# Optimization experiments

Hardware: AMD Instinct MI355X
Metric: run time of the kernel (lower is better)

Reference implementation:

```python
import jax, jax.numpy as jnp
import numpy as np

R = 16
ALPHA = 32
SCALING = ALPHA / R
SLOTS = 32
IN_F = 4096
OUT_F = 4096
B, T = 8, 1024


def setup_inputs() -> dict:
    key = jax.random.key(0)
    k1, k2, k3, k4, k5, k6 = jax.random.split(key, 6)
    x = jax.random.normal(k1, (B, T, IN_F), dtype=jnp.float32)
    adapter_mapping = jax.random.randint(k2, (B,), 0, SLOTS, dtype=jnp.int32)
    W = jax.random.normal(k3, (OUT_F, IN_F), dtype=jnp.float32) * 0.02
    b = jax.random.normal(k4, (OUT_F,), dtype=jnp.float32) * 0.02
    lora_As = jax.random.normal(k5, (SLOTS, IN_F, R), dtype=jnp.float32) * 0.02
    lora_Bs = jax.random.normal(k6, (SLOTS, R, OUT_F), dtype=jnp.float32) * 0.02
    return {"x": x, "adapter_mapping": adapter_mapping, "W": W, "b": b,
            "lora_As": lora_As, "lora_Bs": lora_Bs}


def reference(x, adapter_mapping, W, b, lora_As, lora_Bs):
    # base linear: y = x @ W.T + b
    base_out = jnp.einsum('bti,oi->bto', x, W) + b
    # per-example adapter gather (index_select along slot dim)
    A = lora_As[adapter_mapping]          # [B, in, r]
    Bm = lora_Bs[adapter_mapping]         # [B, r, out]
    lora_h = jnp.einsum('bti,bir->btr', x, A)
    lora_out = jnp.einsum('btr,bro->bto', lora_h, Bm)
    return base_out + lora_out * SCALING
```

## Files before the change

### kernel.cpp

```cpp
#include <hip/hip_runtime.h>
#include <hip/hip_bf16.h>


typedef __bf16 bf16_t;
typedef __bf16 bf16x8 __attribute__((ext_vector_type(8)));
typedef __bf16 bf16x4 __attribute__((ext_vector_type(4)));
typedef float f32x4 __attribute__((ext_vector_type(4)));

#define M_DIM 8192
#define K_DIM 4096
#define N_DIM 4096
#define SCALE_F 2.0f

#define LORA_BLOCKS 256
#define CVT_BLOCKS 2048
#define PREP_BLOCKS (LORA_BLOCKS + CVT_BLOCKS)

__device__ __forceinline__ void gload_lds16(const void* g, void* l) {
    __builtin_amdgcn_global_load_lds(
        (const __attribute__((address_space(1))) void*)g,
        (__attribute__((address_space(3))) void*)l, 16, 0, 0);
}

__global__ __launch_bounds__(256) void prep_kernel(
    const float* __restrict__ X,
    const float* __restrict__ lora_As,
    const int* __restrict__ mapping,
    float* __restrict__ h_ws,
    bf16_t* __restrict__ Xb,
    const float* __restrict__ W,
    bf16_t* __restrict__ Wb)
{
    __shared__ bf16_t Xt[32 * 16 * 8];
    __shared__ bf16_t At[16 * 136];
    __shared__ float hred[4 * 2 * 16 * 16];

    const int tid = threadIdx.x;
    const int bid = blockIdx.x;

    if (bid >= LORA_BLOCKS) {
        if (Wb) {
            const int n4 = N_DIM * K_DIM / 4;
            int i = (bid - LORA_BLOCKS) * 256 + tid;
            const int stride = CVT_BLOCKS * 256;
            for (; i < n4; i += stride) {
                f32x4 v = ((const f32x4*)W)[i];
                bf16x4 o = {(bf16_t)v[0], (bf16_t)v[1], (bf16_t)v[2], (bf16_t)v[3]};
                ((bf16x4*)Wb)[i] = o;
            }
        }
        return;
    }

    const int wave = tid >> 6;
    const int lane = tid & 63;
    const int bm0  = bid * 32;
    const int slot = mapping[bm0 >> 10];
    const float* __restrict__ A = lora_As + (size_t)slot * (K_DIM * 16);

    const int srow = tid >> 3;
    const int sc2  = tid & 7;
    const int r16  = lane & 15;
    const int kq   = lane >> 4;
    const int kk   = tid >> 1;
    const int half = tid & 1;

    f32x4 acc[2];
    acc[0] = (f32x4){0.f, 0.f, 0.f, 0.f};
    acc[1] = (f32x4){0.f, 0.f, 0.f, 0.f};

    const float* xrow = X + (size_t)(bm0 + srow) * K_DIM + sc2 * 16;

    f32x4 xv0 = *(const f32x4*)(xrow);
    f32x4 xv1 = *(const f32x4*)(xrow + 4);
    f32x4 xv2 = *(const f32x4*)(xrow + 8);
    f32x4 xv3 = *(const f32x4*)(xrow + 12);
    f32x4 av0 = *(const f32x4*)(A + (size_t)kk * 16 + half * 8);
    f32x4 av1 = *(const f32x4*)(A + (size_t)kk * 16 + half * 8 + 4);

    for (int k0 = 0; k0 < K_DIM; k0 += 128) {
        bf16x8 c0 = {(bf16_t)xv0[0], (bf16_t)xv0[1], (bf16_t)xv0[2], (bf16_t)xv0[3],
                     (bf16_t)xv1[0], (bf16_t)xv1[1], (bf16_t)xv1[2], (bf16_t)xv1[3]};
        bf16x8 c1 = {(bf16_t)xv2[0], (bf16_t)xv2[1], (bf16_t)xv2[2], (bf16_t)xv2[3],
                     (bf16_t)xv3[0], (bf16_t)xv3[1], (bf16_t)xv3[2], (bf16_t)xv3[3]};
        if (Xb) {
            bf16x8* xbp = (bf16x8*)(Xb + (size_t)(bm0 + srow) * K_DIM + k0 + sc2 * 16);
            xbp[0] = c0;
            xbp[1] = c1;
        }
        const int k8a = sc2 * 2, k8b = sc2 * 2 + 1;
        *(bf16x8*)(Xt + (srow * 16 + (k8a ^ (srow & 15))) * 8) = c0;
        *(bf16x8*)(Xt + (srow * 16 + (k8b ^ (srow & 15))) * 8) = c1;

#pragma unroll
        for (int rr = 0; rr < 4; ++rr) {
            At[(half * 8 + rr) * 136 + kk]     = (bf16_t)av0[rr];
            At[(half * 8 + 4 + rr) * 136 + kk] = (bf16_t)av1[rr];
        }
        __syncthreads();

        if (k0 + 128 < K_DIM) {
            const float* xp = xrow + k0 + 128;
            xv0 = *(const f32x4*)(xp);
            xv1 = *(const f32x4*)(xp + 4);
            xv2 = *(const f32x4*)(xp + 8);
            xv3 = *(const f32x4*)(xp + 12);
            const float* ap = A + (size_t)(k0 + 128 + kk) * 16 + half * 8;
            av0 = *(const f32x4*)ap;
            av1 = *(const f32x4*)(ap + 4);
        }

#pragma unroll
        for (int i = 0; i < 2; ++i) {
            const int row_l = i * 16 + r16;
            const int c = wave * 4 + kq;
            bf16x8 af  = *(const bf16x8*)(Xt + (row_l * 16 + (c ^ (row_l & 15))) * 8);
            bf16x8 bfr = *(const bf16x8*)(At + r16 * 136 + wave * 32 + kq * 8);
            acc[i] = __builtin_amdgcn_mfma_f32_16x16x32_bf16(af, bfr, acc[i], 0, 0, 0);
        }
        __syncthreads();
    }

#pragma unroll
    for (int i = 0; i < 2; ++i)
#pragma unroll
        for (int e = 0; e < 4; ++e)
            hred[wave * 512 + i * 256 + (kq * 4 + e) * 16 + r16] = acc[i][e];
    __syncthreads();
#pragma unroll
    for (int q = 0; q < 2; ++q) {
        const int entry = tid * 2 + q;
        const int row_l = entry >> 4, col = entry & 15;
        const int i = row_l >> 4, rr = row_l & 15;
        const int off = i * 256 + rr * 16 + col;
        float s = hred[off] + hred[512 + off] + hred[1024 + off] + hred[1536 + off];
        h_ws[(size_t)(bm0 + row_l) * 16 + col] = s * SCALE_F;
    }
}

__device__ __forceinline__ void epilogue(
    f32x4 (&acc)[4][4], const float* __restrict__ bias,
    const float* __restrict__ lora_Bs, const int* __restrict__ mapping,
    const float* __restrict__ h_ws, float* __restrict__ out,
    int bm0, int bn0, int wm0, int wn0, int r16, int kq)
{
    const int slot = mapping[bm0 >> 10];
    const bool hasK = (kq < 2);
    const int kq2 = hasK ? kq : 0;

    bf16x8 hfrag[4], bmf[4];
#pragma unroll
    for (int i = 0; i < 4; ++i) {
        const float* hp = h_ws + (size_t)(bm0 + wm0 + i * 16 + r16) * 16 + kq2 * 8;
        f32x4 h0 = *(const f32x4*)hp;
        f32x4 h1 = *(const f32x4*)(hp + 4);
#pragma unroll
        for (int jj = 0; jj < 4; ++jj) {
            hfrag[i][jj]     = hasK ? (bf16_t)h0[jj] : (bf16_t)0.f;
            hfrag[i][jj + 4] = hasK ? (bf16_t)h1[jj] : (bf16_t)0.f;
        }
    }
#pragma unroll
    for (int j = 0; j < 4; ++j) {
        const int o = bn0 + wn0 + j * 16 + r16;
#pragma unroll
        for (int jj = 0; jj < 8; ++jj) {
            const int r = kq2 * 8 + jj;
            const float v = lora_Bs[((size_t)slot * 16 + r) * N_DIM + o];
            bmf[j][jj] = hasK ? (bf16_t)v : (bf16_t)0.f;
        }
    }
#pragma unroll
    for (int i = 0; i < 4; ++i)
#pragma unroll
        for (int j = 0; j < 4; ++j)
            acc[i][j] = __builtin_amdgcn_mfma_f32_16x16x32_bf16(hfrag[i], bmf[j], acc[i][j], 0, 0, 0);

#pragma unroll
    for (int j = 0; j < 4; ++j) {
        const int o = bn0 + wn0 + j * 16 + r16;
        const float bv = bias[o];
#pragma unroll
        for (int i = 0; i < 4; ++i) {
#pragma unroll
            for (int e = 0; e < 4; ++e) {
                const int m = bm0 + wm0 + i * 16 + kq * 4 + e;
                out[(size_t)m * N_DIM + o] = acc[i][j][e] + bv;
            }
        }
    }
}

__global__ __launch_bounds__(256) void gemm_lora_direct(
    const bf16_t* __restrict__ Xb, const bf16_t* __restrict__ Wb,
    const float* __restrict__ bias, const float* __restrict__ lora_Bs,
    const int* __restrict__ mapping, const float* __restrict__ h_ws,
    float* __restrict__ out)
{
    __shared__ bf16_t As[128 * 64];
    __shared__ bf16_t Bs[128 * 64];

    const int tid  = threadIdx.x;
    const int wave = tid >> 6;
    const int lane = tid & 63;
    const int bid  = blockIdx.x;
    const int n_t  = (bid & 7) + ((bid >> 9) << 3);
    const int m_t  = (bid >> 3) & 63;
    const int bm0 = m_t * 128;
    const int bn0 = n_t * 128;
    const int wm0 = (wave >> 1) * 64;
    const int wn0 = (wave & 1) * 64;
    const int r16 = lane & 15;
    const int kq  = lane >> 4;

    f32x4 acc[4][4];
#pragma unroll
    for (int i = 0; i < 4; ++i)
#pragma unroll
        for (int j = 0; j < 4; ++j) acc[i][j] = (f32x4){0.f, 0.f, 0.f, 0.f};

    for (int k0 = 0; k0 < K_DIM; k0 += 64) {
#pragma unroll
        for (int p = 0; p < 4; ++p) {
            const int base = wave * 256 + p * 64;
            const int s    = base + lane;
            const int row  = s >> 3;
            const int k8g  = (s & 7) ^ (row & 7);
            gload_lds16(Xb + (size_t)(bm0 + row) * K_DIM + k0 + k8g * 8,
                        As + (size_t)base * 8);
            gload_lds16(Wb + (size_t)(bn0 + row) * K_DIM + k0 + k8g * 8,
                        Bs + (size_t)base * 8);
        }
        __syncthreads();

#pragma unroll
        for (int kh = 0; kh < 2; ++kh) {
            bf16x8 af[4], bfr[4];
            const int k8 = kh * 4 + kq;
#pragma unroll
            for (int i = 0; i < 4; ++i) {
                const int ra = wm0 + i * 16 + r16;
                const int rb = wn0 + i * 16 + r16;
                af[i]  = *(const bf16x8*)(As + ((size_t)ra * 8 + (k8 ^ (ra & 7))) * 8);
                bfr[i] = *(const bf16x8*)(Bs + ((size_t)rb * 8 + (k8 ^ (rb & 7))) * 8);
            }
#pragma unroll
            for (int i = 0; i < 4; ++i)
#pragma unroll
                for (int j = 0; j < 4; ++j)
                    acc[i][j] = __builtin_amdgcn_mfma_f32_16x16x32_bf16(af[i], bfr[j], acc[i][j], 0, 0, 0);
        }
        __syncthreads();
    }

    epilogue(acc, bias, lora_Bs, mapping, h_ws, out, bm0, bn0, wm0, wn0, r16, kq);
}

__global__ __launch_bounds__(256) void gemm_lora_f32s(
    const float* __restrict__ Xf, const float* __restrict__ Wf,
    const float* __restrict__ bias, const float* __restrict__ lora_Bs,
    const int* __restrict__ mapping, const float* __restrict__ h_ws,
    float* __restrict__ out)
{
    __shared__ float Asf[128 * 32];
    __shared__ float Bsf[128 * 32];

    const int tid  = threadIdx.x;
    const int wave = tid >> 6;
    const int lane = tid & 63;
    const int bid  = blockIdx.x;
    const int n_t  = (bid & 7) + ((bid >> 9) << 3);
    const int m_t  = (bid >> 3) & 63;
    const int bm0 = m_t * 128;
    const int bn0 = n_t * 128;
    const int wm0 = (wave >> 1) * 64;
    const int wn0 = (wave & 1) * 64;
    const int r16 = lane & 15;
    const int kq  = lane >> 4;

    f32x4 acc[4][4];
#pragma unroll
    for (int i = 0; i < 4; ++i)
#pragma unroll
        for (int j = 0; j < 4; ++j) acc[i][j] = (f32x4){0.f, 0.f, 0.f, 0.f};

    for (int k0 = 0; k0 < K_DIM; k0 += 32) {
#pragma unroll
        for (int p = 0; p < 4; ++p) {
            const int idx0 = (p * 4 + wave) * 64;
            const int idx  = idx0 + lane;
            const int k4   = idx >> 7;
            const int row  = idx & 127;
            gload_lds16(Xf + (size_t)(bm0 + row) * K_DIM + (k0 + k4 * 4),
                        Asf + (size_t)idx0 * 4);
            gload_lds16(Wf + (size_t)(bn0 + row) * K_DIM + (k0 + k4 * 4),
                        Bsf + (size_t)idx0 * 4);
        }
        __syncthreads();

        bf16x8 af[4], bfr[4];
#pragma unroll
        for (int i = 0; i < 4; ++i) {
            const int ra = wm0 + i * 16 + r16;
            const int rb = wn0 + i * 16 + r16;
            f32x4 a0 = *(const f32x4*)(Asf + ((size_t)(kq * 2) * 128 + ra) * 4);
            f32x4 a1 = *(const f32x4*)(Asf + ((size_t)(kq * 2 + 1) * 128 + ra) * 4);
            f32x4 b0 = *(const f32x4*)(Bsf + ((size_t)(kq * 2) * 128 + rb) * 4);
            f32x4 b1 = *(const f32x4*)(Bsf + ((size_t)(kq * 2 + 1) * 128 + rb) * 4);
            af[i]  = (bf16x8){(bf16_t)a0[0], (bf16_t)a0[1], (bf16_t)a0[2], (bf16_t)a0[3],
                              (bf16_t)a1[0], (bf16_t)a1[1], (bf16_t)a1[2], (bf16_t)a1[3]};
            bfr[i] = (bf16x8){(bf16_t)b0[0], (bf16_t)b0[1], (bf16_t)b0[2], (bf16_t)b0[3],
                              (bf16_t)b1[0], (bf16_t)b1[1], (bf16_t)b1[2], (bf16_t)b1[3]};
        }
#pragma unroll
        for (int i = 0; i < 4; ++i)
#pragma unroll
            for (int j = 0; j < 4; ++j)
                acc[i][j] = __builtin_amdgcn_mfma_f32_16x16x32_bf16(af[i], bfr[j], acc[i][j], 0, 0, 0);
        __syncthreads();
    }

    epilogue(acc, bias, lora_Bs, mapping, h_ws, out, bm0, bn0, wm0, wn0, r16, kq);
}

extern "C" void kernel_launch(void* const* d_in, const int* in_sizes, int n_in,
                              void* d_out, int out_size, void* d_ws, size_t ws_size,
                              hipStream_t stream) {
    const float* x        = (const float*)d_in[0];
    const int*   mapping  = (const int*)d_in[1];
    const float* W        = (const float*)d_in[2];
    const float* b        = (const float*)d_in[3];
    const float* lora_As  = (const float*)d_in[4];
    const float* lora_Bs  = (const float*)d_in[5];
    float* out = (float*)d_out;

    const size_t xb_bytes = (size_t)M_DIM * K_DIM * 2;
    const size_t wb_bytes = (size_t)N_DIM * K_DIM * 2;
    const size_t h_bytes  = (size_t)M_DIM * 16 * 4;
    const bool direct = ws_size >= xb_bytes + wb_bytes + h_bytes;

    bf16_t* Xb = (bf16_t*)d_ws;
    bf16_t* Wb = (bf16_t*)((char*)d_ws + xb_bytes);
    float*  h_ws = direct ? (float*)((char*)d_ws + xb_bytes + wb_bytes)
                          : (float*)d_ws;

    prep_kernel<<<dim3(PREP_BLOCKS), 256, 0, stream>>>(
        x, lora_As, mapping, h_ws,
        direct ? Xb : nullptr, W, direct ? Wb : nullptr);

    if (direct) {
        gemm_lora_direct<<<dim3(2048), 256, 0, stream>>>(
            Xb, Wb, b, lora_Bs, mapping, h_ws, out);
    } else {
        gemm_lora_f32s<<<dim3(2048), 256, 0, stream>>>(
            x, W, b, lora_Bs, mapping, h_ws, out);
    }
}
```

Before: 721.8 us.

## Split LoRA down-projection over K chunks and launch GEMM in two halves

The LoRA h computation in the prep kernel is split across four K chunks, giving four times as many blocks, and the GEMM epilogue sums the partial h results. Fewer blocks now do the W conversion, and the main GEMM is launched as two kernels, each covering half of the M tiles. The aim is more parallelism in the prep stage, which was limited by long serial K loops in 256 blocks. The cost is extra workspace, extra h loads in the epilogue, and one more kernel launch.

```diff
diff --git a/kernel.cpp b/kernel.cpp
--- a/kernel.cpp
+++ b/kernel.cpp
@@ -12,9 +12,7 @@
 #define N_DIM 4096
 #define SCALE_F 2.0f
 
-#define LORA_BLOCKS 256
-#define CVT_BLOCKS 2048
-#define PREP_BLOCKS (LORA_BLOCKS + CVT_BLOCKS)
+#define CVT_BLOCKS 1024
 
 __device__ __forceinline__ void gload_lds16(const void* g, void* l) {
     __builtin_amdgcn_global_load_lds(
@@ -29,7 +27,8 @@
     float* __restrict__ h_ws,
     bf16_t* __restrict__ Xb,
     const float* __restrict__ W,
-    bf16_t* __restrict__ Wb)
+    bf16_t* __restrict__ Wb,
+    int lora_blocks, int kshift)
 {
     __shared__ bf16_t Xt[32 * 16 * 8];
     __shared__ bf16_t At[16 * 136];
@@ -38,11 +37,11 @@
     const int tid = threadIdx.x;
     const int bid = blockIdx.x;
 
-    if (bid >= LORA_BLOCKS) {
+    if (bid >= lora_blocks) {
         if (Wb) {
             const int n4 = N_DIM * K_DIM / 4;
-            int i = (bid - LORA_BLOCKS) * 256 + tid;
-            const int stride = CVT_BLOCKS * 256;
+            int i = (bid - lora_blocks) * 256 + tid;
+            const int stride = (gridDim.x - lora_blocks) * 256;
             for (; i < n4; i += stride) {
                 f32x4 v = ((const f32x4*)W)[i];
                 bf16x4 o = {(bf16_t)v[0], (bf16_t)v[1], (bf16_t)v[2], (bf16_t)v[3]};
@@ -52,9 +51,15 @@
         return;
     }
 
+    const int kcn    = 1 << kshift;
+    const int mchunk = bid >> kshift;
+    const int kc     = bid & (kcn - 1);
+    const int kspan  = K_DIM >> kshift;
+    const int kbeg   = kc * kspan;
+
     const int wave = tid >> 6;
     const int lane = tid & 63;
-    const int bm0  = bid * 32;
+    const int bm0  = mchunk * 32;
     const int slot = mapping[bm0 >> 10];
     const float* __restrict__ A = lora_As + (size_t)slot * (K_DIM * 16);
 
@@ -71,14 +76,14 @@
 
     const float* xrow = X + (size_t)(bm0 + srow) * K_DIM + sc2 * 16;
 
-    f32x4 xv0 = *(const f32x4*)(xrow);
-    f32x4 xv1 = *(const f32x4*)(xrow + 4);
-    f32x4 xv2 = *(const f32x4*)(xrow + 8);
-    f32x4 xv3 = *(const f32x4*)(xrow + 12);
-    f32x4 av0 = *(const f32x4*)(A + (size_t)kk * 16 + half * 8);
-    f32x4 av1 = *(const f32x4*)(A + (size_t)kk * 16 + half * 8 + 4);
-
-    for (int k0 = 0; k0 < K_DIM; k0 += 128) {
+    f32x4 xv0 = *(const f32x4*)(xrow + kbeg);
+    f32x4 xv1 = *(const f32x4*)(xrow + kbeg + 4);
+    f32x4 xv2 = *(const f32x4*)(xrow + kbeg + 8);
+    f32x4 xv3 = *(const f32x4*)(xrow + kbeg + 12);
+    f32x4 av0 = *(const f32x4*)(A + (size_t)(kbeg + kk) * 16 + half * 8);
+    f32x4 av1 = *(const f32x4*)(A + (size_t)(kbeg + kk) * 16 + half * 8 + 4);
+
+    for (int k0 = kbeg; k0 < kbeg + kspan; k0 += 128) {
         bf16x8 c0 = {(bf16_t)xv0[0], (bf16_t)xv0[1], (bf16_t)xv0[2], (bf16_t)xv0[3],
                      (bf16_t)xv1[0], (bf16_t)xv1[1], (bf16_t)xv1[2], (bf16_t)xv1[3]};
         bf16x8 c1 = {(bf16_t)xv2[0], (bf16_t)xv2[1], (bf16_t)xv2[2], (bf16_t)xv2[3],
@@ -99,7 +104,7 @@
         }
         __syncthreads();
 
-        if (k0 + 128 < K_DIM) {
+        if (k0 + 128 < kbeg + kspan) {
             const float* xp = xrow + k0 + 128;
             xv0 = *(const f32x4*)(xp);
             xv1 = *(const f32x4*)(xp + 4);
@@ -127,6 +132,7 @@
         for (int e = 0; e < 4; ++e)
             hred[wave * 512 + i * 256 + (kq * 4 + e) * 16 + r16] = acc[i][e];
     __syncthreads();
+    float* hout = h_ws + (size_t)kc * (M_DIM * 16);
 #pragma unroll
     for (int q = 0; q < 2; ++q) {
         const int entry = tid * 2 + q;
@@ -134,14 +140,14 @@
         const int i = row_l >> 4, rr = row_l & 15;
         const int off = i * 256 + rr * 16 + col;
         float s = hred[off] + hred[512 + off] + hred[1024 + off] + hred[1536 + off];
-        h_ws[(size_t)(bm0 + row_l) * 16 + col] = s * SCALE_F;
+        hout[(size_t)(bm0 + row_l) * 16 + col] = s * SCALE_F;
     }
 }
 
 __device__ __forceinline__ void epilogue(
     f32x4 (&acc)[4][4], const float* __restrict__ bias,
     const float* __restrict__ lora_Bs, const int* __restrict__ mapping,
-    const float* __restrict__ h_ws, float* __restrict__ out,
+    const float* __restrict__ h_ws, int kcn, float* __restrict__ out,
     int bm0, int bn0, int wm0, int wn0, int r16, int kq)
 {
     const int slot = mapping[bm0 >> 10];
@@ -154,6 +160,11 @@
         const float* hp = h_ws + (size_t)(bm0 + wm0 + i * 16 + r16) * 16 + kq2 * 8;
         f32x4 h0 = *(const f32x4*)hp;
         f32x4 h1 = *(const f32x4*)(hp + 4);
+        for (int c = 1; c < kcn; ++c) {
+            const float* hq = hp + (size_t)c * (M_DIM * 16);
+            h0 += *(const f32x4*)hq;
+            h1 += *(const f32x4*)(hq + 4);
+        }
 #pragma unroll
         for (int jj = 0; jj < 4; ++jj) {
             hfrag[i][jj]     = hasK ? (bf16_t)h0[jj] : (bf16_t)0.f;
@@ -194,11 +205,76 @@
 __global__ __launch_bounds__(256) void gemm_lora_direct(
     const bf16_t* __restrict__ Xb, const bf16_t* __restrict__ Wb,
     const float* __restrict__ bias, const float* __restrict__ lora_Bs,
+    const int* __restrict__ mapping, const float* __restrict__ h_ws, int kcn,
+    float* __restrict__ out, int m_base)
+{
+    __shared__ bf16_t As[128 * 64];
+    __shared__ bf16_t Bs[128 * 64];
+
+    const int tid  = threadIdx.x;
+    const int wave = tid >> 6;
+    const int lane = tid & 63;
+    const int bid  = blockIdx.x;
+    const int n_t  = (bid & 7) + ((bid >> 8) << 3);
+    const int m_t  = ((bid >> 3) & 31) + m_base;
+    const int bm0 = m_t * 128;
+    const int bn0 = n_t * 128;
+    const int wm0 = (wave >> 1) * 64;
+    const int wn0 = (wave & 1) * 64;
+    const int r16 = lane & 15;
+    const int kq  = lane >> 4;
+
+    f32x4 acc[4][4];
+#pragma unroll
+    for (int i = 0; i < 4; ++i)
+#pragma unroll
+        for (int j = 0; j < 4; ++j) acc[i][j] = (f32x4){0.f, 0.f, 0.f, 0.f};
+
+    for (int k0 = 0; k0 < K_DIM; k0 += 64) {
+#pragma unroll
+        for (int p = 0; p < 4; ++p) {
+            const int base = wave * 256 + p * 64;
+            const int s    = base + lane;
+            const int row  = s >> 3;
+            const int k8g  = (s & 7) ^ (row & 7);
+            gload_lds16(Xb + (size_t)(bm0 + row) * K_DIM + k0 + k8g * 8,
+                        As + (size_t)base * 8);
+            gload_lds16(Wb + (size_t)(bn0 + row) * K_DIM + k0 + k8g * 8,
+                        Bs + (size_t)base * 8);
+        }
+        __syncthreads();
+
+#pragma unroll
+        for (int kh = 0; kh < 2; ++kh) {
+            bf16x8 af[4], bfr[4];
+            const int k8 = kh * 4 + kq;
+#pragma unroll
+            for (int i = 0; i < 4; ++i) {
+                const int ra = wm0 + i * 16 + r16;
+                const int rb = wn0 + i * 16 + r16;
+                af[i]  = *(const bf16x8*)(As + ((size_t)ra * 8 + (k8 ^ (ra & 7))) * 8);
+                bfr[i] = *(const bf16x8*)(Bs + ((size_t)rb * 8 + (k8 ^ (rb & 7))) * 8);
+            }
+#pragma unroll
+            for (int i = 0; i < 4; ++i)
+#pragma unroll
+                for (int j = 0; j < 4; ++j)
+                    acc[i][j] = __builtin_amdgcn_mfma_f32_16x16x32_bf16(af[i], bfr[j], acc[i][j], 0, 0, 0);
+        }
+        __syncthreads();
+    }
+
+    epilogue(acc, bias, lora_Bs, mapping, h_ws, kcn, out, bm0, bn0, wm0, wn0, r16, kq);
+}
+
+__global__ __launch_bounds__(256) void gemm_lora_f32s(
+    const float* __restrict__ Xf, const float* __restrict__ Wf,
+    const float* __restrict__ bias, const float* __restrict__ lora_Bs,
     const int* __restrict__ mapping, const float* __restrict__ h_ws,
     float* __restrict__ out)
 {
-    __shared__ bf16_t As[128 * 64];
-    __shared__ bf16_t Bs[128 * 64];
+    __shared__ float Asf[128 * 32];
+    __shared__ float Bsf[128 * 32];
 
     const int tid  = threadIdx.x;
     const int wave = tid >> 6;
@@ -219,71 +295,6 @@
 #pragma unroll
         for (int j = 0; j < 4; ++j) acc[i][j] = (f32x4){0.f, 0.f, 0.f, 0.f};
 
-    for (int k0 = 0; k0 < K_DIM; k0 += 64) {
-#pragma unroll
-        for (int p = 0; p < 4; ++p) {
-            const int base = wave * 256 + p * 64;
-            const int s    = base + lane;
-            const int row  = s >> 3;
-            const int k8g  = (s & 7) ^ (row & 7);
-            gload_lds16(Xb + (size_t)(bm0 + row) * K_DIM + k0 + k8g * 8,
-                        As + (size_t)base * 8);
-            gload_lds16(Wb + (size_t)(bn0 + row) * K_DIM + k0 + k8g * 8,
-                        Bs + (size_t)base * 8);
-        }
-        __syncthreads();
-
-#pragma unroll
-        for (int kh = 0; kh < 2; ++kh) {
-            bf16x8 af[4], bfr[4];
-            const int k8 = kh * 4 + kq;
-#pragma unroll
-            for (int i = 0; i < 4; ++i) {
-                const int ra = wm0 + i * 16 + r16;
-                const int rb = wn0 + i * 16 + r16;
-                af[i]  = *(const bf16x8*)(As + ((size_t)ra * 8 + (k8 ^ (ra & 7))) * 8);
-                bfr[i] = *(const bf16x8*)(Bs + ((size_t)rb * 8 + (k8 ^ (rb & 7))) * 8);
-            }
-#pragma unroll
-            for (int i = 0; i < 4; ++i)
-#pragma unroll
-                for (int j = 0; j < 4; ++j)
-                    acc[i][j] = __builtin_amdgcn_mfma_f32_16x16x32_bf16(af[i], bfr[j], acc[i][j], 0, 0, 0);
-        }
-        __syncthreads();
-    }
-
-    epilogue(acc, bias, lora_Bs, mapping, h_ws, out, bm0, bn0, wm0, wn0, r16, kq);
-}
-
-__global__ __launch_bounds__(256) void gemm_lora_f32s(
-    const float* __restrict__ Xf, const float* __restrict__ Wf,
-    const float* __restrict__ bias, const float* __restrict__ lora_Bs,
-    const int* __restrict__ mapping, const float* __restrict__ h_ws,
-    float* __restrict__ out)
-{
-    __shared__ float Asf[128 * 32];
-    __shared__ float Bsf[128 * 32];
-
-    const int tid  = threadIdx.x;
-    const int wave = tid >> 6;
-    const int lane = tid & 63;
-    const int bid  = blockIdx.x;
-    const int n_t  = (bid & 7) + ((bid >> 9) << 3);
-    const int m_t  = (bid >> 3) & 63;
-    const int bm0 = m_t * 128;
-    const int bn0 = n_t * 128;
-    const int wm0 = (wave >> 1) * 64;
-    const int wn0 = (wave & 1) * 64;
-    const int r16 = lane & 15;
-    const int kq  = lane >> 4;
-
-    f32x4 acc[4][4];
-#pragma unroll
-    for (int i = 0; i < 4; ++i)
-#pragma unroll
-        for (int j = 0; j < 4; ++j) acc[i][j] = (f32x4){0.f, 0.f, 0.f, 0.f};
-
     for (int k0 = 0; k0 < K_DIM; k0 += 32) {
 #pragma unroll
         for (int p = 0; p < 4; ++p) {
@@ -320,7 +331,7 @@
         __syncthreads();
     }
 
-    epilogue(acc, bias, lora_Bs, mapping, h_ws, out, bm0, bn0, wm0, wn0, r16, kq);
+    epilogue(acc, bias, lora_Bs, mapping, h_ws, 1, out, bm0, bn0, wm0, wn0, r16, kq);
 }
 
 extern "C" void kernel_launch(void* const* d_in, const int* in_sizes, int n_in,
@@ -337,21 +348,28 @@
     const size_t xb_bytes = (size_t)M_DIM * K_DIM * 2;
     const size_t wb_bytes = (size_t)N_DIM * K_DIM * 2;
     const size_t h_bytes  = (size_t)M_DIM * 16 * 4;
-    const bool direct = ws_size >= xb_bytes + wb_bytes + h_bytes;
+    const bool direct4 = ws_size >= xb_bytes + wb_bytes + 4 * h_bytes;
+    const bool direct1 = ws_size >= xb_bytes + wb_bytes + h_bytes;
 
     bf16_t* Xb = (bf16_t*)d_ws;
     bf16_t* Wb = (bf16_t*)((char*)d_ws + xb_bytes);
-    float*  h_ws = direct ? (float*)((char*)d_ws + xb_bytes + wb_bytes)
-                          : (float*)d_ws;
-
-    prep_kernel<<<dim3(PREP_BLOCKS), 256, 0, stream>>>(
-        x, lora_As, mapping, h_ws,
-        direct ? Xb : nullptr, W, direct ? Wb : nullptr);
-
-    if (direct) {
-        gemm_lora_direct<<<dim3(2048), 256, 0, stream>>>(
-            Xb, Wb, b, lora_Bs, mapping, h_ws, out);
+
+    if (direct4 || direct1) {
+        const int kshift = direct4 ? 2 : 0;
+        const int kcn    = 1 << kshift;
+        const int lora_blocks = 256 * kcn;
+        float* h_ws = (float*)((char*)d_ws + xb_bytes + wb_bytes);
+
+        prep_kernel<<<dim3(lora_blocks + CVT_BLOCKS), 256, 0, stream>>>(
+            x, lora_As, mapping, h_ws, Xb, W, Wb, lora_blocks, kshift);
+        gemm_lora_direct<<<dim3(1024), 256, 0, stream>>>(
+            Xb, Wb, b, lora_Bs, mapping, h_ws, kcn, out, 0);
+        gemm_lora_direct<<<dim3(1024), 256, 0, stream>>>(
+            Xb, Wb, b, lora_Bs, mapping, h_ws, kcn, out, 32);
     } else {
+        float* h_ws = (float*)d_ws;
+        prep_kernel<<<dim3(256 + CVT_BLOCKS), 256, 0, stream>>>(
+            x, lora_As, mapping, h_ws, nullptr, W, nullptr, 256, 0);
         gemm_lora_f32s<<<dim3(2048), 256, 0, stream>>>(
             x, W, b, lora_Bs, mapping, h_ws, out);
     }
```

Result: faster. 643.1 us (-10.9%).
